# Performance work log

Measured on AMD Instinct MI355X. Metric: run time of the kernel, lower is better.

The kernel has to match this reference:

```python
import jax, jax.numpy as jnp
import numpy as np

B, T, F, H = 64, 2048, 256, 512


def setup_inputs() -> dict:
    key = jax.random.key(0)
    ks = jax.random.split(key, 8)
    s_ih = 1.0 / np.sqrt(H)
    return {
        "z": jax.random.normal(ks[0], (B, H), dtype=jnp.float32),
        "x": jax.random.normal(ks[1], (B, T, F), dtype=jnp.float32),
        "W_ih": jax.random.uniform(ks[2], (4 * H, F), minval=-s_ih, maxval=s_ih, dtype=jnp.float32),
        "W_hh": jax.random.uniform(ks[3], (4 * H, H), minval=-s_ih, maxval=s_ih, dtype=jnp.float32),
        "b_ih": jax.random.uniform(ks[4], (4 * H,), minval=-s_ih, maxval=s_ih, dtype=jnp.float32),
        "b_hh": jax.random.uniform(ks[5], (4 * H,), minval=-s_ih, maxval=s_ih, dtype=jnp.float32),
        "W_lin": jax.random.uniform(ks[6], (F, H), minval=-s_ih, maxval=s_ih, dtype=jnp.float32),
        "b_lin": jax.random.uniform(ks[7], (F,), minval=-s_ih, maxval=s_ih, dtype=jnp.float32),
    }


def _lstm_decode(z, x, W_ih, W_hh, b_ih, b_hh, W_lin, b_lin):
    # Teacher forcing: cell input at step t is x[:, t]. h0 = z, c0 = 0.
    # Precompute input projections for all timesteps in one GEMM: [T, B, 4H]
    x_t_major = jnp.swapaxes(x, 0, 1)  # [T, B, F]
    x_proj = jnp.einsum("tbf,gf->tbg", x_t_major, W_ih) + (b_ih + b_hh)
    h0 = z
    c0 = jnp.zeros_like(z)

    def step(carry, xp):
        h, c = carry
        gates = xp + h @ W_hh.T  # [B, 4H]
        i, f, g, o = jnp.split(gates, 4, axis=-1)  # PyTorch gate order: i,f,g,o
        i = jax.nn.sigmoid(i)
        f = jax.nn.sigmoid(f)
        g = jnp.tanh(g)
        o = jax.nn.sigmoid(o)
        c_new = f * c + i * g
        h_new = o * jnp.tanh(c_new)
        out_t = h_new @ W_lin.T + b_lin  # [B, F]
        return (h_new, c_new), out_t

    _, outs = jax.lax.scan(step, (h0, c0), x_proj)  # outs: [T, B, F]
    return jnp.swapaxes(outs, 0, 1)  # [B, T, F]


def reference(z, x, W_ih, W_hh, b_ih, b_hh, W_lin, b_lin):
    return _lstm_decode(z, x, W_ih, W_hh, b_ih, b_hh, W_lin, b_lin)
```

## Files before the change

### kernel.cpp

```cpp
#include <hip/hip_runtime.h>
#include <hip/hip_bf16.h>

#define B_   64
#define T_   2048
#define F_   256
#define H_   512
#define GB   4
#define GG   8
#define NWG  (GB*GG)
#define PKTS_PER_GROUP 4096
#define SLOTS 4

typedef __attribute__((ext_vector_type(8))) short bfrag;
typedef __attribute__((ext_vector_type(4))) int   int4v;
typedef __attribute__((ext_vector_type(2))) int   int2v;
typedef __attribute__((ext_vector_type(4))) float f32x4;
typedef __attribute__((ext_vector_type(4))) float float4_t;

__device__ __forceinline__ float fsig(float x)  { return 1.0f / (1.0f + __expf(-x)); }
__device__ __forceinline__ float ftanh(float x) { return 2.0f / (1.0f + __expf(-2.0f * x)) - 1.0f; }
__device__ __forceinline__ short f2bf(float f) {
  __hip_bfloat16 h = __float2bfloat16(f);
  return __builtin_bit_cast(short, h);
}

__device__ __forceinline__ int2v gload8_cc(const void* p) {
  int2v r;
  asm volatile("global_load_dwordx2 %0, %1, off sc0 sc1" : "=v"(r) : "v"(p));
  return r;
}
__device__ __forceinline__ void gstore8_cc(void* p, int2v d) {
  asm volatile("global_store_dwordx2 %0, %1, off sc0 sc1" :: "v"(p), "v"(d));
}
__device__ __forceinline__ void vm_drain() {
  asm volatile("s_waitcnt vmcnt(0)" ::: "memory");
  __builtin_amdgcn_sched_barrier(0);
}

__global__ void lstm_init(const float* __restrict__ z, unsigned long long* __restrict__ pkt0) {
  int i = blockIdx.x * blockDim.x + threadIdx.x;
  int g  = i >> 12;
  int p  = i & 4095;
  int j  = p >> 8;
  int pr = p & 255;
  int row = 16 * g + j;
  unsigned int lo = (unsigned)(unsigned short)f2bf(z[(size_t)row * H_ + 2 * pr])
                  | ((unsigned)(unsigned short)f2bf(z[(size_t)row * H_ + 2 * pr + 1]) << 16);
  pkt0[i] = (unsigned long long)lo;
}

__global__ void __launch_bounds__(256, 1)
lstm_persist(const float* __restrict__ x,
             const float* __restrict__ Wih,  const float* __restrict__ Whh,
             const float* __restrict__ bih,  const float* __restrict__ bhh,
             const float* __restrict__ Wlin, const float* __restrict__ blin,
             float* __restrict__ out, int2v* __restrict__ pkt)
{
  __shared__ char smem[49152];

  const int wg  = blockIdx.x;
  const int b   = wg >> 3;
  const int k   = wg & 7;
  const int tid = threadIdx.x;
  const int wv  = tid >> 6;
  const int l   = tid & 63;
  const int l16 = l & 15;
  const int qq  = l >> 4;
  const int swz = (l16 & 7) << 4;
  const int m4  = qq << 2;

  {
    const int oc = tid >> 3;
    const float* src = Wlin + (size_t)(32 * k + oc) * H_ + (tid & 7) * 64;
    char* dst = smem + 16384 + oc * 1024;
    #pragma unroll
    for (int i = 0; i < 8; ++i) {
      bfrag tmp;
      #pragma unroll
      for (int e = 0; e < 8; ++e) tmp[e] = f2bf(src[i * 8 + e]);
      *(int4v*)(dst + ((((tid & 7) * 128) + i * 16) ^ ((oc & 7) << 4))) =
          __builtin_bit_cast(int4v, tmp);
    }
  }

  bfrag WH[4][16];
  bfrag WI[4][8];
  float bs[4];
  #pragma unroll
  for (int q = 0; q < 4; ++q) {
    const int grow = q * H_ + k * 64 + wv * 16 + l16;
    #pragma unroll
    for (int kt = 0; kt < 16; ++kt) {
      const float* s = Whh + (size_t)grow * H_ + kt * 32 + qq * 8;
      bfrag w;
      #pragma unroll
      for (int e = 0; e < 8; ++e) w[e] = f2bf(s[e]);
      WH[q][kt] = w;
    }
    #pragma unroll
    for (int kt = 0; kt < 8; ++kt) {
      const float* s = Wih + (size_t)grow * F_ + kt * 32 + qq * 8;
      bfrag w;
      #pragma unroll
      for (int e = 0; e < 8; ++e) w[e] = f2bf(s[e]);
      WI[q][kt] = w;
    }
    bs[q] = bih[grow] + bhh[grow];
  }
  const float blc = (wv < 2) ? blin[32 * k + 16 * wv + l16] : 0.f;

  float c4[4] = {0.f, 0.f, 0.f, 0.f};
  __syncthreads();

  for (int t = 0; t < T_; ++t) {
    f32x4 acc[4] = {{0,0,0,0},{0,0,0,0},{0,0,0,0},{0,0,0,0}};
    {
      const float* xr = x + ((size_t)(16 * b + l16) * T_ + t) * F_ + qq * 8;
      #pragma unroll
      for (int kt = 0; kt < 8; ++kt) {
        float4_t xa = *(const float4_t*)(xr + kt * 32);
        float4_t xb = *(const float4_t*)(xr + kt * 32 + 4);
        bfrag a;
        #pragma unroll
        for (int e = 0; e < 4; ++e) { a[e] = f2bf(xa[e]); a[4 + e] = f2bf(xb[e]); }
        #pragma unroll
        for (int q = 0; q < 4; ++q)
          acc[q] = __builtin_amdgcn_mfma_f32_16x16x32_bf16(a, WI[q][kt], acc[q], 0, 0, 0);
      }
    }

    const int2v* pp = pkt + (size_t)((t & 3) * GB + b) * PKTS_PER_GROUP + tid;
    int2v pv[16];
    while (true) {
      #pragma unroll
      for (int j = 0; j < 16; ++j) pv[j] = gload8_cc(pp + j * 256);
      vm_drain();
      bool ok = true;
      #pragma unroll
      for (int j = 0; j < 16; ++j) ok &= (pv[j].y == t);
      if (__all(ok)) break;
      __builtin_amdgcn_s_sleep(2);
    }
    __syncthreads();

    #pragma unroll
    for (int j = 0; j < 16; ++j)
      *(int*)(smem + j * 1024 + ((tid * 4) ^ ((j & 7) << 4))) = pv[j].x;
    __syncthreads();

    f32x4 oacc = {blc, blc, blc, blc};
    #pragma unroll
    for (int kt = 0; kt < 16; ++kt) {
      bfrag a = *(const bfrag*)(smem + l16 * 1024 + ((kt * 64 + qq * 16) ^ swz));
      #pragma unroll
      for (int q = 0; q < 4; ++q)
        acc[q] = __builtin_amdgcn_mfma_f32_16x16x32_bf16(a, WH[q][kt], acc[q], 0, 0, 0);
      if (wv < 2) {
        bfrag wl = *(const bfrag*)(smem + 16384 + (16 * wv + l16) * 1024 +
                                   ((kt * 64 + qq * 16) ^ swz));
        oacc = __builtin_amdgcn_mfma_f32_16x16x32_bf16(a, wl, oacc, 0, 0, 0);
      }
    }

    int2v* ps = pkt + (size_t)(((t + 1) & 3) * GB + b) * PKTS_PER_GROUP;
    #pragma unroll
    for (int r = 0; r < 4; ++r) {
      float iv = fsig(acc[0][r] + bs[0]);
      float fv = fsig(acc[1][r] + bs[1]);
      float gv = ftanh(acc[2][r] + bs[2]);
      float ov = fsig(acc[3][r] + bs[3]);
      float cn = fv * c4[r] + iv * gv;
      c4[r] = cn;
      float hn = ov * ftanh(cn);
      int hb = (int)(unsigned short)f2bf(hn);
      int pu = __shfl_xor(hb, 1);
      if ((l16 & 1) == 0) {
        int2v pk;
        pk.x = (hb & 0xffff) | (pu << 16);
        pk.y = t + 1;
        gstore8_cc(ps + (m4 + r) * 256 + (32 * k + 8 * wv + (l16 >> 1)), pk);
      }
    }

    if (t > 0 && wv < 2) {
      #pragma unroll
      for (int r = 0; r < 4; ++r)
        out[(size_t)(16 * b + m4 + r) * T_ * F_ + (size_t)(t - 1) * F_ +
            32 * k + 16 * wv + l16] = oacc[r];
    }
  }

  {
    const int2v* pp = pkt + (size_t)((T_ & 3) * GB + b) * PKTS_PER_GROUP + tid;
    int2v pv[16];
    while (true) {
      #pragma unroll
      for (int j = 0; j < 16; ++j) pv[j] = gload8_cc(pp + j * 256);
      vm_drain();
      bool ok = true;
      #pragma unroll
      for (int j = 0; j < 16; ++j) ok &= (pv[j].y == T_);
      if (__all(ok)) break;
      __builtin_amdgcn_s_sleep(2);
    }
    __syncthreads();
    #pragma unroll
    for (int j = 0; j < 16; ++j)
      *(int*)(smem + j * 1024 + ((tid * 4) ^ ((j & 7) << 4))) = pv[j].x;
    __syncthreads();

    if (wv < 2) {
      f32x4 oacc = {blc, blc, blc, blc};
      #pragma unroll
      for (int kt = 0; kt < 16; ++kt) {
        bfrag a  = *(const bfrag*)(smem + l16 * 1024 + ((kt * 64 + qq * 16) ^ swz));
        bfrag wl = *(const bfrag*)(smem + 16384 + (16 * wv + l16) * 1024 +
                                   ((kt * 64 + qq * 16) ^ swz));
        oacc = __builtin_amdgcn_mfma_f32_16x16x32_bf16(a, wl, oacc, 0, 0, 0);
      }
      #pragma unroll
      for (int r = 0; r < 4; ++r)
        out[(size_t)(16 * b + m4 + r) * T_ * F_ + (size_t)(T_ - 1) * F_ +
            32 * k + 16 * wv + l16] = oacc[r];
    }
  }
}

extern "C" void kernel_launch(void* const* d_in, const int* in_sizes, int n_in,
                              void* d_out, int out_size, void* d_ws, size_t ws_size,
                              hipStream_t stream) {
  const float* z    = (const float*)d_in[0];
  const float* x    = (const float*)d_in[1];
  const float* Wih  = (const float*)d_in[2];
  const float* Whh  = (const float*)d_in[3];
  const float* bih  = (const float*)d_in[4];
  const float* bhh  = (const float*)d_in[5];
  const float* Wlin = (const float*)d_in[6];
  const float* blin = (const float*)d_in[7];
  float* out = (float*)d_out;

  int2v* pkt = (int2v*)d_ws;

  lstm_init<<<64, 256, 0, stream>>>(z, (unsigned long long*)d_ws);
  lstm_persist<<<NWG, 256, 0, stream>>>(x, Wih, Whh, bih, bhh, Wlin, blin, out, pkt);
}
```

Before: 14.19 ms.

## Regroup workgroups by XCD and exchange hidden state through L2 when co-located

The persistent LSTM grid moves from 32 workgroups (4 batch groups of 16 rows) to 64 workgroups (8 batch groups of 8 rows). Each group of 8 workgroups shares one hidden-state exchange. At startup every workgroup publishes its XCD id and checks whether its group peers sit on the same XCD. If they do, it polls a second packet buffer with L2-scope loads instead of system-coherent ones, to cut the latency of each step's cross-workgroup handoff. Every packet is now written to both buffers, half the MFMA rows are wasted padding, and a timeout falls back to the slow path.

```diff
diff --git a/kernel.cpp b/kernel.cpp
--- a/kernel.cpp
+++ b/kernel.cpp
@@ -5,10 +5,10 @@
 #define T_   2048
 #define F_   256
 #define H_   512
-#define GB   4
-#define GG   8
-#define NWG  (GB*GG)
-#define PKTS_PER_GROUP 4096
+#define NG   8
+#define GR   8
+#define NWG  64
+#define PKTS 2048
 #define SLOTS 4
 
 typedef __attribute__((ext_vector_type(8))) short bfrag;
@@ -32,21 +32,44 @@
 __device__ __forceinline__ void gstore8_cc(void* p, int2v d) {
   asm volatile("global_store_dwordx2 %0, %1, off sc0 sc1" :: "v"(p), "v"(d));
 }
+__device__ __forceinline__ void gstore4_cc(void* p, int d) {
+  asm volatile("global_store_dword %0, %1, off sc0 sc1" :: "v"(p), "v"(d));
+}
+__device__ __forceinline__ int gload_flag(const void* p) {
+  int r;
+  asm volatile("global_load_dword %0, %1, off sc0 sc1\n\ts_waitcnt vmcnt(0)"
+               : "=v"(r) : "v"(p) : "memory");
+  return r;
+}
+__device__ __forceinline__ int2v gload8_l2(const void* p) {
+  int2v r;
+  asm volatile("global_load_dwordx2 %0, %1, off sc0" : "=v"(r) : "v"(p));
+  return r;
+}
+__device__ __forceinline__ void gstore8_l2(void* p, int2v d) {
+  asm volatile("global_store_dwordx2 %0, %1, off sc0" :: "v"(p), "v"(d));
+}
 __device__ __forceinline__ void vm_drain() {
   asm volatile("s_waitcnt vmcnt(0)" ::: "memory");
   __builtin_amdgcn_sched_barrier(0);
 }
 
-__global__ void lstm_init(const float* __restrict__ z, unsigned long long* __restrict__ pkt0) {
+__global__ void lstm_init(const float* __restrict__ z,
+                          unsigned long long* __restrict__ fast0,
+                          unsigned long long* __restrict__ slow0,
+                          int* __restrict__ xcdmap) {
   int i = blockIdx.x * blockDim.x + threadIdx.x;
-  int g  = i >> 12;
-  int p  = i & 4095;
-  int j  = p >> 8;
-  int pr = p & 255;
-  int row = 16 * g + j;
+  if (i < NWG) xcdmap[i] = -1;
+  int g  = i >> 11;
+  int P  = i & 2047;
+  int r  = P >> 8;
+  int pr = P & 255;
+  int row = g * GR + r;
   unsigned int lo = (unsigned)(unsigned short)f2bf(z[(size_t)row * H_ + 2 * pr])
                   | ((unsigned)(unsigned short)f2bf(z[(size_t)row * H_ + 2 * pr + 1]) << 16);
-  pkt0[i] = (unsigned long long)lo;
+  unsigned long long pk = (unsigned long long)lo;
+  fast0[(size_t)g * PKTS + P] = pk;
+  slow0[(size_t)g * PKTS + P] = pk;
 }
 
 __global__ void __launch_bounds__(256, 1)
@@ -54,25 +77,44 @@
              const float* __restrict__ Wih,  const float* __restrict__ Whh,
              const float* __restrict__ bih,  const float* __restrict__ bhh,
              const float* __restrict__ Wlin, const float* __restrict__ blin,
-             float* __restrict__ out, int2v* __restrict__ pkt)
+             float* __restrict__ out,
+             int2v* __restrict__ fastp, int2v* __restrict__ slowp,
+             int* __restrict__ xcdmap)
 {
-  __shared__ char smem[49152];
+  __shared__ char smem[8192 + 32768 + 16];
+  const int hOff = 0, wOff = 8192, fOff = 8192 + 32768;
 
   const int wg  = blockIdx.x;
-  const int b   = wg >> 3;
-  const int k   = wg & 7;
+  const int g   = wg & 7;
+  const int mem = wg >> 3;
   const int tid = threadIdx.x;
   const int wv  = tid >> 6;
   const int l   = tid & 63;
   const int l16 = l & 15;
   const int qq  = l >> 4;
-  const int swz = (l16 & 7) << 4;
-  const int m4  = qq << 2;
+
+  const int xcc = __builtin_amdgcn_s_getreg(6164);
+  if (tid == 0) gstore4_cc(&xcdmap[wg], xcc);
+  vm_drain();
+  if (wv == 0) {
+    int other = xcc;
+    bool got = (l >= NG);
+    for (int it = 0; it < 200000; ++it) {
+      if (!got) {
+        int v = gload_flag(&xcdmap[g + NG * l]);
+        if (v != -1) { other = v; got = true; }
+      }
+      if (__all(got)) break;
+      __builtin_amdgcn_s_sleep(1);
+    }
+    int ok = __all(got && (other == xcc)) ? 1 : 0;
+    if (l == 0) *(int*)(smem + fOff) = ok;
+  }
 
   {
     const int oc = tid >> 3;
-    const float* src = Wlin + (size_t)(32 * k + oc) * H_ + (tid & 7) * 64;
-    char* dst = smem + 16384 + oc * 1024;
+    const float* src = Wlin + (size_t)(32 * mem + oc) * H_ + (tid & 7) * 64;
+    char* dst = smem + wOff + oc * 1024;
     #pragma unroll
     for (int i = 0; i < 8; ++i) {
       bfrag tmp;
@@ -83,12 +125,11 @@
     }
   }
 
-  bfrag WH[4][16];
-  bfrag WI[4][8];
+  bfrag WH[4][16], WI[4][8];
   float bs[4];
   #pragma unroll
   for (int q = 0; q < 4; ++q) {
-    const int grow = q * H_ + k * 64 + wv * 16 + l16;
+    const int grow = q * H_ + 64 * mem + 16 * wv + l16;
     #pragma unroll
     for (int kt = 0; kt < 16; ++kt) {
       const float* s = Whh + (size_t)grow * H_ + kt * 32 + qq * 8;
@@ -107,15 +148,18 @@
     }
     bs[q] = bih[grow] + bhh[grow];
   }
-  const float blc = (wv < 2) ? blin[32 * k + 16 * wv + l16] : 0.f;
+  const float blc = (wv < 2) ? blin[32 * mem + 16 * wv + l16] : 0.f;
 
   float c4[4] = {0.f, 0.f, 0.f, 0.f};
   __syncthreads();
+  bool useFast = (*(int*)(smem + fOff) != 0);
+
+  const int P0 = (tid >> 5) * 256 + (tid & 31);
 
   for (int t = 0; t < T_; ++t) {
     f32x4 acc[4] = {{0,0,0,0},{0,0,0,0},{0,0,0,0},{0,0,0,0}};
     {
-      const float* xr = x + ((size_t)(16 * b + l16) * T_ + t) * F_ + qq * 8;
+      const float* xr = x + ((size_t)(GR * g + (l16 & 7)) * T_ + t) * F_ + qq * 8;
       #pragma unroll
       for (int kt = 0; kt < 8; ++kt) {
         float4_t xa = *(const float4_t*)(xr + kt * 32);
@@ -129,99 +173,138 @@
       }
     }
 
-    const int2v* pp = pkt + (size_t)((t & 3) * GB + b) * PKTS_PER_GROUP + tid;
-    int2v pv[16];
+    const size_t slotOff = (size_t)((t & 3) * NG + g) * PKTS;
+    const int2v* fb = fastp + slotOff + P0;
+    const int2v* sb = slowp + slotOff + P0;
+    int2v pv[8];
+    int iter = 0;
     while (true) {
-      #pragma unroll
-      for (int j = 0; j < 16; ++j) pv[j] = gload8_cc(pp + j * 256);
+      if (useFast) {
+        #pragma unroll
+        for (int j = 0; j < 8; ++j) pv[j] = gload8_l2(fb + 32 * j);
+      } else {
+        #pragma unroll
+        for (int j = 0; j < 8; ++j) pv[j] = gload8_cc(sb + 32 * j);
+      }
       vm_drain();
       bool ok = true;
       #pragma unroll
-      for (int j = 0; j < 16; ++j) ok &= (pv[j].y == t);
+      for (int j = 0; j < 8; ++j) ok &= (pv[j].y == t);
       if (__all(ok)) break;
-      __builtin_amdgcn_s_sleep(2);
+      if (useFast && ++iter > 30000) useFast = false;
+      __builtin_amdgcn_s_sleep(1);
     }
     __syncthreads();
 
-    #pragma unroll
-    for (int j = 0; j < 16; ++j)
-      *(int*)(smem + j * 1024 + ((tid * 4) ^ ((j & 7) << 4))) = pv[j].x;
+    {
+      const int r = tid >> 5;
+      char* base = smem + hOff + r * 1024;
+      #pragma unroll
+      for (int j = 0; j < 8; ++j)
+        *(int*)(base + ((4 * ((tid & 31) + 32 * j)) ^ ((r & 7) << 4))) = pv[j].x;
+    }
     __syncthreads();
 
     f32x4 oacc = {blc, blc, blc, blc};
     #pragma unroll
     for (int kt = 0; kt < 16; ++kt) {
-      bfrag a = *(const bfrag*)(smem + l16 * 1024 + ((kt * 64 + qq * 16) ^ swz));
+      bfrag a = *(const bfrag*)(smem + hOff + (l16 & 7) * 1024 +
+                                ((kt * 64 + qq * 16) ^ ((l16 & 7) << 4)));
       #pragma unroll
       for (int q = 0; q < 4; ++q)
         acc[q] = __builtin_amdgcn_mfma_f32_16x16x32_bf16(a, WH[q][kt], acc[q], 0, 0, 0);
       if (wv < 2) {
-        bfrag wl = *(const bfrag*)(smem + 16384 + (16 * wv + l16) * 1024 +
-                                   ((kt * 64 + qq * 16) ^ swz));
+        const int oc = 16 * wv + l16;
+        bfrag wl = *(const bfrag*)(smem + wOff + oc * 1024 +
+                                   ((kt * 64 + qq * 16) ^ ((oc & 7) << 4)));
         oacc = __builtin_amdgcn_mfma_f32_16x16x32_bf16(a, wl, oacc, 0, 0, 0);
       }
     }
 
-    int2v* ps = pkt + (size_t)(((t + 1) & 3) * GB + b) * PKTS_PER_GROUP;
+    const size_t nxtOff = (size_t)(((t + 1) & 3) * NG + g) * PKTS;
+    int2v* fs = fastp + nxtOff;
+    int2v* ss = slowp + nxtOff;
     #pragma unroll
     for (int r = 0; r < 4; ++r) {
-      float iv = fsig(acc[0][r] + bs[0]);
-      float fv = fsig(acc[1][r] + bs[1]);
-      float gv = ftanh(acc[2][r] + bs[2]);
-      float ov = fsig(acc[3][r] + bs[3]);
-      float cn = fv * c4[r] + iv * gv;
-      c4[r] = cn;
-      float hn = ov * ftanh(cn);
+      float hn = 0.f;
+      if (qq < 2) {
+        float iv = fsig(acc[0][r] + bs[0]);
+        float fv = fsig(acc[1][r] + bs[1]);
+        float gv = ftanh(acc[2][r] + bs[2]);
+        float ov = fsig(acc[3][r] + bs[3]);
+        float cn = fv * c4[r] + iv * gv;
+        c4[r] = cn;
+        hn = ov * ftanh(cn);
+      }
       int hb = (int)(unsigned short)f2bf(hn);
       int pu = __shfl_xor(hb, 1);
-      if ((l16 & 1) == 0) {
+      if (qq < 2 && (l16 & 1) == 0) {
         int2v pk;
         pk.x = (hb & 0xffff) | (pu << 16);
         pk.y = t + 1;
-        gstore8_cc(ps + (m4 + r) * 256 + (32 * k + 8 * wv + (l16 >> 1)), pk);
-      }
-    }
-
-    if (t > 0 && wv < 2) {
+        const int P = (4 * qq + r) * 256 + (32 * mem + 8 * wv + (l16 >> 1));
+        gstore8_l2(fs + P, pk);
+        gstore8_cc(ss + P, pk);
+      }
+    }
+
+    if (t > 0 && wv < 2 && qq < 2) {
       #pragma unroll
       for (int r = 0; r < 4; ++r)
-        out[(size_t)(16 * b + m4 + r) * T_ * F_ + (size_t)(t - 1) * F_ +
-            32 * k + 16 * wv + l16] = oacc[r];
+        out[(size_t)(GR * g + 4 * qq + r) * T_ * F_ + (size_t)(t - 1) * F_ +
+            32 * mem + 16 * wv + l16] = oacc[r];
     }
   }
 
   {
-    const int2v* pp = pkt + (size_t)((T_ & 3) * GB + b) * PKTS_PER_GROUP + tid;
-    int2v pv[16];
+    const size_t slotOff = (size_t)((T_ & 3) * NG + g) * PKTS;
+    const int2v* fb = fastp + slotOff + P0;
+    const int2v* sb = slowp + slotOff + P0;
+    int2v pv[8];
+    int iter = 0;
     while (true) {
-      #pragma unroll
-      for (int j = 0; j < 16; ++j) pv[j] = gload8_cc(pp + j * 256);
+      if (useFast) {
+        #pragma unroll
+        for (int j = 0; j < 8; ++j) pv[j] = gload8_l2(fb + 32 * j);
+      } else {
+        #pragma unroll
+        for (int j = 0; j < 8; ++j) pv[j] = gload8_cc(sb + 32 * j);
+      }
       vm_drain();
       bool ok = true;
       #pragma unroll
-      for (int j = 0; j < 16; ++j) ok &= (pv[j].y == T_);
+      for (int j = 0; j < 8; ++j) ok &= (pv[j].y == T_);
       if (__all(ok)) break;
-      __builtin_amdgcn_s_sleep(2);
+      if (useFast && ++iter > 30000) useFast = false;
+      __builtin_amdgcn_s_sleep(1);
     }
     __syncthreads();
-    #pragma unroll
-    for (int j = 0; j < 16; ++j)
-      *(int*)(smem + j * 1024 + ((tid * 4) ^ ((j & 7) << 4))) = pv[j].x;
+    {
+      const int r = tid >> 5;
+      char* base = smem + hOff + r * 1024;
+      #pragma unroll
+      for (int j = 0; j < 8; ++j)
+        *(int*)(base + ((4 * ((tid & 31) + 32 * j)) ^ ((r & 7) << 4))) = pv[j].x;
+    }
     __syncthreads();
 
     if (wv < 2) {
       f32x4 oacc = {blc, blc, blc, blc};
       #pragma unroll
       for (int kt = 0; kt < 16; ++kt) {
-        bfrag a  = *(const bfrag*)(smem + l16 * 1024 + ((kt * 64 + qq * 16) ^ swz));
-        bfrag wl = *(const bfrag*)(smem + 16384 + (16 * wv + l16) * 1024 +
-                                   ((kt * 64 + qq * 16) ^ swz));
+        bfrag a = *(const bfrag*)(smem + hOff + (l16 & 7) * 1024 +
+                                  ((kt * 64 + qq * 16) ^ ((l16 & 7) << 4)));
+        const int oc = 16 * wv + l16;
+        bfrag wl = *(const bfrag*)(smem + wOff + oc * 1024 +
+                                   ((kt * 64 + qq * 16) ^ ((oc & 7) << 4)));
         oacc = __builtin_amdgcn_mfma_f32_16x16x32_bf16(a, wl, oacc, 0, 0, 0);
       }
-      #pragma unroll
-      for (int r = 0; r < 4; ++r)
-        out[(size_t)(16 * b + m4 + r) * T_ * F_ + (size_t)(T_ - 1) * F_ +
-            32 * k + 16 * wv + l16] = oacc[r];
+      if (qq < 2) {
+        #pragma unroll
+        for (int r = 0; r < 4; ++r)
+          out[(size_t)(GR * g + 4 * qq + r) * T_ * F_ + (size_t)(T_ - 1) * F_ +
+              32 * mem + 16 * wv + l16] = oacc[r];
+      }
     }
   }
 }
@@ -239,8 +322,13 @@
   const float* blin = (const float*)d_in[7];
   float* out = (float*)d_out;
 
-  int2v* pkt = (int2v*)d_ws;
-
-  lstm_init<<<64, 256, 0, stream>>>(z, (unsigned long long*)d_ws);
-  lstm_persist<<<NWG, 256, 0, stream>>>(x, Wih, Whh, bih, bhh, Wlin, blin, out, pkt);
-}
+  const size_t bufBytes = (size_t)SLOTS * NG * PKTS * 8;
+  int2v* fastp = (int2v*)d_ws;
+  int2v* slowp = (int2v*)((char*)d_ws + bufBytes);
+  int*   xcdmap = (int*)((char*)d_ws + 2 * bufBytes);
+
+  lstm_init<<<64, 256, 0, stream>>>(z, (unsigned long long*)fastp,
+                                    (unsigned long long*)slowp, xcdmap);
+  lstm_persist<<<NWG, 256, 0, stream>>>(x, Wih, Whh, bih, bhh, Wlin, blin, out,
+                                        fastp, slowp, xcdmap);
+}
```

Result: slower. 38.70 ms (+172.8%).

## Replace per-packet sequence tags with per-workgroup flags and double-buffered payload

Applied to the files above, without the earlier changes.

Swaps the inter-workgroup handoff of the hidden state, which tagged every 8-byte packet with a step number and polled all packets, for 4-byte payload writes plus one flag per workgroup written after a drain and block barrier. Consumers spin on 8 flags and then read the payload once, which halves the payload traffic and shrinks polling to a few small loads. The ring drops from 4 slots to 2. In exchange it adds an extra vm drain, a __syncthreads and a serialized flag store on every step, and the release ordering rests on sc0/sc1 stores being visible before the flag.

```diff
diff --git a/kernel.cpp b/kernel.cpp
--- a/kernel.cpp
+++ b/kernel.cpp
@@ -8,12 +8,10 @@
 #define GB   4
 #define GG   8
 #define NWG  (GB*GG)
-#define PKTS_PER_GROUP 4096
-#define SLOTS 4
+#define PAYD 4096
 
 typedef __attribute__((ext_vector_type(8))) short bfrag;
 typedef __attribute__((ext_vector_type(4))) int   int4v;
-typedef __attribute__((ext_vector_type(2))) int   int2v;
 typedef __attribute__((ext_vector_type(4))) float f32x4;
 typedef __attribute__((ext_vector_type(4))) float float4_t;
 
@@ -24,29 +22,37 @@
   return __builtin_bit_cast(short, h);
 }
 
-__device__ __forceinline__ int2v gload8_cc(const void* p) {
-  int2v r;
-  asm volatile("global_load_dwordx2 %0, %1, off sc0 sc1" : "=v"(r) : "v"(p));
+__device__ __forceinline__ int gload4_cc(const void* p) {
+  int r;
+  asm volatile("global_load_dword %0, %1, off sc0 sc1" : "=v"(r) : "v"(p));
   return r;
 }
-__device__ __forceinline__ void gstore8_cc(void* p, int2v d) {
-  asm volatile("global_store_dwordx2 %0, %1, off sc0 sc1" :: "v"(p), "v"(d));
+__device__ __forceinline__ void gstore4_cc(void* p, int d) {
+  asm volatile("global_store_dword %0, %1, off sc0 sc1" :: "v"(p), "v"(d));
+}
+__device__ __forceinline__ int gload_flag(const void* p) {
+  int r;
+  asm volatile("global_load_dword %0, %1, off sc0 sc1\n\ts_waitcnt vmcnt(0)"
+               : "=v"(r) : "v"(p) : "memory");
+  return r;
 }
 __device__ __forceinline__ void vm_drain() {
   asm volatile("s_waitcnt vmcnt(0)" ::: "memory");
   __builtin_amdgcn_sched_barrier(0);
 }
 
-__global__ void lstm_init(const float* __restrict__ z, unsigned long long* __restrict__ pkt0) {
+__global__ void lstm_init(const float* __restrict__ z, int* __restrict__ pay,
+                          int* __restrict__ flags) {
   int i = blockIdx.x * blockDim.x + threadIdx.x;
+  if (i < GB * 16) flags[i] = 0;
   int g  = i >> 12;
   int p  = i & 4095;
   int j  = p >> 8;
   int pr = p & 255;
   int row = 16 * g + j;
-  unsigned int lo = (unsigned)(unsigned short)f2bf(z[(size_t)row * H_ + 2 * pr])
-                  | ((unsigned)(unsigned short)f2bf(z[(size_t)row * H_ + 2 * pr + 1]) << 16);
-  pkt0[i] = (unsigned long long)lo;
+  int lo = (int)((unsigned)(unsigned short)f2bf(z[(size_t)row * H_ + 2 * pr])
+         | ((unsigned)(unsigned short)f2bf(z[(size_t)row * H_ + 2 * pr + 1]) << 16));
+  pay[(size_t)g * PAYD + p] = lo;
 }
 
 __global__ void __launch_bounds__(256, 1)
@@ -54,7 +60,8 @@
              const float* __restrict__ Wih,  const float* __restrict__ Whh,
              const float* __restrict__ bih,  const float* __restrict__ bhh,
              const float* __restrict__ Wlin, const float* __restrict__ blin,
-             float* __restrict__ out, int2v* __restrict__ pkt)
+             float* __restrict__ out, int* __restrict__ pay,
+             int* __restrict__ flags)
 {
   __shared__ char smem[49152];
 
@@ -112,6 +119,8 @@
   float c4[4] = {0.f, 0.f, 0.f, 0.f};
   __syncthreads();
 
+  const int* myflags = flags + b * 16;
+
   for (int t = 0; t < T_; ++t) {
     f32x4 acc[4] = {{0,0,0,0},{0,0,0,0},{0,0,0,0},{0,0,0,0}};
     {
@@ -129,23 +138,24 @@
       }
     }
 
-    const int2v* pp = pkt + (size_t)((t & 3) * GB + b) * PKTS_PER_GROUP + tid;
-    int2v pv[16];
-    while (true) {
-      #pragma unroll
-      for (int j = 0; j < 16; ++j) pv[j] = gload8_cc(pp + j * 256);
-      vm_drain();
-      bool ok = true;
-      #pragma unroll
-      for (int j = 0; j < 16; ++j) ok &= (pv[j].y == t);
-      if (__all(ok)) break;
-      __builtin_amdgcn_s_sleep(2);
-    }
+    if (t > 0) {
+      while (true) {
+        int v = gload_flag(&myflags[l & 7]);
+        if (__all(v >= t)) break;
+        __builtin_amdgcn_s_sleep(1);
+      }
+      __builtin_amdgcn_sched_barrier(0);
+    }
+    const int* pp = pay + (size_t)((t & 1) * GB + b) * PAYD + tid;
+    int pv[16];
+    #pragma unroll
+    for (int j = 0; j < 16; ++j) pv[j] = gload4_cc(pp + j * 256);
+    vm_drain();
     __syncthreads();
 
     #pragma unroll
     for (int j = 0; j < 16; ++j)
-      *(int*)(smem + j * 1024 + ((tid * 4) ^ ((j & 7) << 4))) = pv[j].x;
+      *(int*)(smem + j * 1024 + ((tid * 4) ^ ((j & 7) << 4))) = pv[j];
     __syncthreads();
 
     f32x4 oacc = {blc, blc, blc, blc};
@@ -162,7 +172,7 @@
       }
     }
 
-    int2v* ps = pkt + (size_t)(((t + 1) & 3) * GB + b) * PKTS_PER_GROUP;
+    int* ps = pay + (size_t)(((t + 1) & 1) * GB + b) * PAYD;
     #pragma unroll
     for (int r = 0; r < 4; ++r) {
       float iv = fsig(acc[0][r] + bs[0]);
@@ -175,12 +185,14 @@
       int hb = (int)(unsigned short)f2bf(hn);
       int pu = __shfl_xor(hb, 1);
       if ((l16 & 1) == 0) {
-        int2v pk;
-        pk.x = (hb & 0xffff) | (pu << 16);
-        pk.y = t + 1;
-        gstore8_cc(ps + (m4 + r) * 256 + (32 * k + 8 * wv + (l16 >> 1)), pk);
-      }
-    }
+        int packed = (hb & 0xffff) | (pu << 16);
+        gstore4_cc(ps + (m4 + r) * 256 + (32 * k + 8 * wv + (l16 >> 1)), packed);
+      }
+    }
+    vm_drain();
+    __syncthreads();
+    if (tid == 0)
+      gstore4_cc((void*)&flags[b * 16 + k], t + 1);
 
     if (t > 0 && wv < 2) {
       #pragma unroll
@@ -191,22 +203,22 @@
   }
 
   {
-    const int2v* pp = pkt + (size_t)((T_ & 3) * GB + b) * PKTS_PER_GROUP + tid;
-    int2v pv[16];
     while (true) {
-      #pragma unroll
-      for (int j = 0; j < 16; ++j) pv[j] = gload8_cc(pp + j * 256);
-      vm_drain();
-      bool ok = true;
-      #pragma unroll
-      for (int j = 0; j < 16; ++j) ok &= (pv[j].y == T_);
-      if (__all(ok)) break;
-      __builtin_amdgcn_s_sleep(2);
-    }
+      int v = gload_flag(&myflags[l & 7]);
+      if (__all(v >= T_)) break;
+      __builtin_amdgcn_s_sleep(1);
+    }
+    __builtin_amdgcn_sched_barrier(0);
+
+    const int* pp = pay + (size_t)((T_ & 1) * GB + b) * PAYD + tid;
+    int pv[16];
+    #pragma unroll
+    for (int j = 0; j < 16; ++j) pv[j] = gload4_cc(pp + j * 256);
+    vm_drain();
     __syncthreads();
     #pragma unroll
     for (int j = 0; j < 16; ++j)
-      *(int*)(smem + j * 1024 + ((tid * 4) ^ ((j & 7) << 4))) = pv[j].x;
+      *(int*)(smem + j * 1024 + ((tid * 4) ^ ((j & 7) << 4))) = pv[j];
     __syncthreads();
 
     if (wv < 2) {
@@ -239,8 +251,10 @@
   const float* blin = (const float*)d_in[7];
   float* out = (float*)d_out;
 
-  int2v* pkt = (int2v*)d_ws;
-
-  lstm_init<<<64, 256, 0, stream>>>(z, (unsigned long long*)d_ws);
-  lstm_persist<<<NWG, 256, 0, stream>>>(x, Wih, Whh, bih, bhh, Wlin, blin, out, pkt);
-}
+  int* pay   = (int*)d_ws;
+  int* flags = (int*)((char*)d_ws + 192 * 1024);
+
+  lstm_init<<<64, 256, 0, stream>>>(z, pay, flags);
+  lstm_persist<<<NWG, 256, 0, stream>>>(x, Wih, Whh, bih, bhh, Wlin, blin, out,
+                                        pay, flags);
+}
```

New measurement: 14.17 ms. No clear change (-0.1%).

## Split recurrent K-reduction across two wave halves and overlap polling with input GEMM

Applied to the files above, without the earlier changes.

Each workgroup goes from 256 to 512 threads. The two halves of the waves each take half of the K dimension for the input and recurrent MFMAs, and the partial sums are reduced through LDS. Gate math runs on one half while the other half computes the output projection, so the output linear no longer sits on the critical path of the gate waves. The packet loads for h are issued before the x-projection MFMAs to hide polling latency. This shortens the per-step serial chain and halves per-thread weight registers, at the cost of an extra LDS reduction and barrier each step.

```diff
diff --git a/kernel.cpp b/kernel.cpp
--- a/kernel.cpp
+++ b/kernel.cpp
@@ -8,8 +8,7 @@
 #define GB   4
 #define GG   8
 #define NWG  (GB*GG)
-#define PKTS_PER_GROUP 4096
-#define SLOTS 4
+#define PAYD 4096
 
 typedef __attribute__((ext_vector_type(8))) short bfrag;
 typedef __attribute__((ext_vector_type(4))) int   int4v;
@@ -37,87 +36,95 @@
   __builtin_amdgcn_sched_barrier(0);
 }
 
-__global__ void lstm_init(const float* __restrict__ z, unsigned long long* __restrict__ pkt0) {
+__global__ void lstm_init(const float* __restrict__ z,
+                          unsigned long long* __restrict__ pkt0) {
   int i = blockIdx.x * blockDim.x + threadIdx.x;
   int g  = i >> 12;
   int p  = i & 4095;
-  int j  = p >> 8;
+  int r  = p >> 8;
   int pr = p & 255;
-  int row = 16 * g + j;
+  int row = 16 * g + r;
   unsigned int lo = (unsigned)(unsigned short)f2bf(z[(size_t)row * H_ + 2 * pr])
                   | ((unsigned)(unsigned short)f2bf(z[(size_t)row * H_ + 2 * pr + 1]) << 16);
-  pkt0[i] = (unsigned long long)lo;
-}
-
-__global__ void __launch_bounds__(256, 1)
+  pkt0[(size_t)g * PAYD + p] = (unsigned long long)lo;
+}
+
+__global__ void __launch_bounds__(512, 1)
 lstm_persist(const float* __restrict__ x,
              const float* __restrict__ Wih,  const float* __restrict__ Whh,
              const float* __restrict__ bih,  const float* __restrict__ bhh,
              const float* __restrict__ Wlin, const float* __restrict__ blin,
              float* __restrict__ out, int2v* __restrict__ pkt)
 {
-  __shared__ char smem[49152];
+  __shared__ char smem[65536];
 
   const int wg  = blockIdx.x;
   const int b   = wg >> 3;
   const int k   = wg & 7;
   const int tid = threadIdx.x;
-  const int wv  = tid >> 6;
+  const int w   = tid >> 6;
+  const int ct  = w & 3;
+  const int kh  = w >> 2;
   const int l   = tid & 63;
   const int l16 = l & 15;
   const int qq  = l >> 4;
+  const int m4  = qq << 2;
   const int swz = (l16 & 7) << 4;
-  const int m4  = qq << 2;
 
   {
-    const int oc = tid >> 3;
-    const float* src = Wlin + (size_t)(32 * k + oc) * H_ + (tid & 7) * 64;
+    const int oc = tid >> 4;
+    const int s  = tid & 15;
+    const float* src = Wlin + (size_t)(32 * k + oc) * H_ + s * 32;
     char* dst = smem + 16384 + oc * 1024;
     #pragma unroll
-    for (int i = 0; i < 8; ++i) {
+    for (int i = 0; i < 4; ++i) {
       bfrag tmp;
       #pragma unroll
       for (int e = 0; e < 8; ++e) tmp[e] = f2bf(src[i * 8 + e]);
-      *(int4v*)(dst + ((((tid & 7) * 128) + i * 16) ^ ((oc & 7) << 4))) =
+      *(int4v*)(dst + ((s * 64 + i * 16) ^ ((oc & 7) << 4))) =
           __builtin_bit_cast(int4v, tmp);
     }
   }
 
-  bfrag WH[4][16];
-  bfrag WI[4][8];
-  float bs[4];
+  bfrag WH[4][8]; bfrag WI[4][4]; float bs[4];
   #pragma unroll
   for (int q = 0; q < 4; ++q) {
-    const int grow = q * H_ + k * 64 + wv * 16 + l16;
-    #pragma unroll
-    for (int kt = 0; kt < 16; ++kt) {
-      const float* s = Whh + (size_t)grow * H_ + kt * 32 + qq * 8;
-      bfrag w;
-      #pragma unroll
-      for (int e = 0; e < 8; ++e) w[e] = f2bf(s[e]);
-      WH[q][kt] = w;
-    }
-    #pragma unroll
-    for (int kt = 0; kt < 8; ++kt) {
-      const float* s = Wih + (size_t)grow * F_ + kt * 32 + qq * 8;
-      bfrag w;
-      #pragma unroll
-      for (int e = 0; e < 8; ++e) w[e] = f2bf(s[e]);
-      WI[q][kt] = w;
+    const int grow = q * H_ + k * 64 + ct * 16 + l16;
+    #pragma unroll
+    for (int kt2 = 0; kt2 < 8; ++kt2) {
+      const float* s = Whh + (size_t)grow * H_ + (8 * kh + kt2) * 32 + qq * 8;
+      bfrag wv_;
+      #pragma unroll
+      for (int e = 0; e < 8; ++e) wv_[e] = f2bf(s[e]);
+      WH[q][kt2] = wv_;
+    }
+    #pragma unroll
+    for (int kt2 = 0; kt2 < 4; ++kt2) {
+      const float* s = Wih + (size_t)grow * F_ + (4 * kh + kt2) * 32 + qq * 8;
+      bfrag wv_;
+      #pragma unroll
+      for (int e = 0; e < 8; ++e) wv_[e] = f2bf(s[e]);
+      WI[q][kt2] = wv_;
     }
     bs[q] = bih[grow] + bhh[grow];
   }
-  const float blc = (wv < 2) ? blin[32 * k + 16 * wv + l16] : 0.f;
+  const float blc = (kh == 1 && ct < 2) ? blin[32 * k + 16 * ct + l16] : 0.f;
 
   float c4[4] = {0.f, 0.f, 0.f, 0.f};
   __syncthreads();
 
   for (int t = 0; t < T_; ++t) {
+    const int2v* pp = pkt + (size_t)((t & 3) * GB + b) * PAYD + tid;
+    int2v pv[8];
+    #pragma unroll
+    for (int j = 0; j < 8; ++j) pv[j] = gload8_cc(pp + j * 512);
+
     f32x4 acc[4] = {{0,0,0,0},{0,0,0,0},{0,0,0,0},{0,0,0,0}};
     {
       const float* xr = x + ((size_t)(16 * b + l16) * T_ + t) * F_ + qq * 8;
       #pragma unroll
-      for (int kt = 0; kt < 8; ++kt) {
+      for (int kt2 = 0; kt2 < 4; ++kt2) {
+        const int kt = 4 * kh + kt2;
         float4_t xa = *(const float4_t*)(xr + kt * 32);
         float4_t xb = *(const float4_t*)(xr + kt * 32 + 4);
         bfrag a;
@@ -125,103 +132,128 @@
         for (int e = 0; e < 4; ++e) { a[e] = f2bf(xa[e]); a[4 + e] = f2bf(xb[e]); }
         #pragma unroll
         for (int q = 0; q < 4; ++q)
-          acc[q] = __builtin_amdgcn_mfma_f32_16x16x32_bf16(a, WI[q][kt], acc[q], 0, 0, 0);
-      }
-    }
-
-    const int2v* pp = pkt + (size_t)((t & 3) * GB + b) * PKTS_PER_GROUP + tid;
-    int2v pv[16];
+          acc[q] = __builtin_amdgcn_mfma_f32_16x16x32_bf16(a, WI[q][kt2], acc[q], 0, 0, 0);
+      }
+    }
+
+    vm_drain();
+    {
+      bool ok = true;
+      #pragma unroll
+      for (int j = 0; j < 8; ++j) ok &= (pv[j].y == t);
+      while (!__all(ok)) {
+        __builtin_amdgcn_s_sleep(2);
+        #pragma unroll
+        for (int j = 0; j < 8; ++j) pv[j] = gload8_cc(pp + j * 512);
+        vm_drain();
+        ok = true;
+        #pragma unroll
+        for (int j = 0; j < 8; ++j) ok &= (pv[j].y == t);
+      }
+    }
+    __syncthreads();
+
+    #pragma unroll
+    for (int j = 0; j < 8; ++j) {
+      const int P = tid + j * 512;
+      *(int*)(smem + (P >> 8) * 1024 + (((P & 255) * 4) ^ (((P >> 8) & 7) << 4))) = pv[j].x;
+    }
+    __syncthreads();
+
+    #pragma unroll
+    for (int kt2 = 0; kt2 < 8; ++kt2) {
+      const int kt = 8 * kh + kt2;
+      bfrag a = *(const bfrag*)(smem + l16 * 1024 + ((kt * 64 + qq * 16) ^ swz));
+      #pragma unroll
+      for (int q = 0; q < 4; ++q)
+        acc[q] = __builtin_amdgcn_mfma_f32_16x16x32_bf16(a, WH[q][kt2], acc[q], 0, 0, 0);
+    }
+
+    if (kh == 1) {
+      #pragma unroll
+      for (int q = 0; q < 4; ++q)
+        *(f32x4*)(smem + 49152 + ct * 4096 + q * 1024 + l * 16) = acc[q];
+    }
+    __syncthreads();
+
+    if (kh == 0) {
+      #pragma unroll
+      for (int q = 0; q < 4; ++q)
+        acc[q] += *(const f32x4*)(smem + 49152 + ct * 4096 + q * 1024 + l * 16);
+
+      int2v* ps = pkt + (size_t)(((t + 1) & 3) * GB + b) * PAYD;
+      #pragma unroll
+      for (int r = 0; r < 4; ++r) {
+        float iv = fsig(acc[0][r] + bs[0]);
+        float fv = fsig(acc[1][r] + bs[1]);
+        float gv = ftanh(acc[2][r] + bs[2]);
+        float ov = fsig(acc[3][r] + bs[3]);
+        float cn = fv * c4[r] + iv * gv;
+        c4[r] = cn;
+        float hn = ov * ftanh(cn);
+        int hb = (int)(unsigned short)f2bf(hn);
+        int pu = __shfl_xor(hb, 1);
+        if ((l16 & 1) == 0) {
+          int2v pk;
+          pk.x = (hb & 0xffff) | (pu << 16);
+          pk.y = t + 1;
+          gstore8_cc(ps + (m4 + r) * 256 + (32 * k + 8 * ct + (l16 >> 1)), pk);
+        }
+      }
+    } else if (ct < 2) {
+      f32x4 oacc = {blc, blc, blc, blc};
+      const int oc = 16 * ct + l16;
+      #pragma unroll
+      for (int kt = 0; kt < 16; ++kt) {
+        bfrag a  = *(const bfrag*)(smem + l16 * 1024 + ((kt * 64 + qq * 16) ^ swz));
+        bfrag wl = *(const bfrag*)(smem + 16384 + oc * 1024 +
+                                   ((kt * 64 + qq * 16) ^ ((oc & 7) << 4)));
+        oacc = __builtin_amdgcn_mfma_f32_16x16x32_bf16(a, wl, oacc, 0, 0, 0);
+      }
+      if (t > 0) {
+        #pragma unroll
+        for (int r = 0; r < 4; ++r)
+          out[(size_t)(16 * b + m4 + r) * T_ * F_ + (size_t)(t - 1) * F_ +
+              32 * k + 16 * ct + l16] = oacc[r];
+      }
+    }
+  }
+
+  {
+    const int2v* pp = pkt + (size_t)((T_ & 3) * GB + b) * PAYD + tid;
+    int2v pv[8];
     while (true) {
       #pragma unroll
-      for (int j = 0; j < 16; ++j) pv[j] = gload8_cc(pp + j * 256);
+      for (int j = 0; j < 8; ++j) pv[j] = gload8_cc(pp + j * 512);
       vm_drain();
       bool ok = true;
       #pragma unroll
-      for (int j = 0; j < 16; ++j) ok &= (pv[j].y == t);
+      for (int j = 0; j < 8; ++j) ok &= (pv[j].y == T_);
       if (__all(ok)) break;
       __builtin_amdgcn_s_sleep(2);
     }
     __syncthreads();
-
-    #pragma unroll
-    for (int j = 0; j < 16; ++j)
-      *(int*)(smem + j * 1024 + ((tid * 4) ^ ((j & 7) << 4))) = pv[j].x;
-    __syncthreads();
-
-    f32x4 oacc = {blc, blc, blc, blc};
-    #pragma unroll
-    for (int kt = 0; kt < 16; ++kt) {
-      bfrag a = *(const bfrag*)(smem + l16 * 1024 + ((kt * 64 + qq * 16) ^ swz));
-      #pragma unroll
-      for (int q = 0; q < 4; ++q)
-        acc[q] = __builtin_amdgcn_mfma_f32_16x16x32_bf16(a, WH[q][kt], acc[q], 0, 0, 0);
-      if (wv < 2) {
-        bfrag wl = *(const bfrag*)(smem + 16384 + (16 * wv + l16) * 1024 +
-                                   ((kt * 64 + qq * 16) ^ swz));
-        oacc = __builtin_amdgcn_mfma_f32_16x16x32_bf16(a, wl, oacc, 0, 0, 0);
-      }
-    }
-
-    int2v* ps = pkt + (size_t)(((t + 1) & 3) * GB + b) * PKTS_PER_GROUP;
-    #pragma unroll
-    for (int r = 0; r < 4; ++r) {
-      float iv = fsig(acc[0][r] + bs[0]);
-      float fv = fsig(acc[1][r] + bs[1]);
-      float gv = ftanh(acc[2][r] + bs[2]);
-      float ov = fsig(acc[3][r] + bs[3]);
-      float cn = fv * c4[r] + iv * gv;
-      c4[r] = cn;
-      float hn = ov * ftanh(cn);
-      int hb = (int)(unsigned short)f2bf(hn);
-      int pu = __shfl_xor(hb, 1);
-      if ((l16 & 1) == 0) {
-        int2v pk;
-        pk.x = (hb & 0xffff) | (pu << 16);
-        pk.y = t + 1;
-        gstore8_cc(ps + (m4 + r) * 256 + (32 * k + 8 * wv + (l16 >> 1)), pk);
-      }
-    }
-
-    if (t > 0 && wv < 2) {
-      #pragma unroll
-      for (int r = 0; r < 4; ++r)
-        out[(size_t)(16 * b + m4 + r) * T_ * F_ + (size_t)(t - 1) * F_ +
-            32 * k + 16 * wv + l16] = oacc[r];
-    }
-  }
-
-  {
-    const int2v* pp = pkt + (size_t)((T_ & 3) * GB + b) * PKTS_PER_GROUP + tid;
-    int2v pv[16];
-    while (true) {
-      #pragma unroll
-      for (int j = 0; j < 16; ++j) pv[j] = gload8_cc(pp + j * 256);
-      vm_drain();
-      bool ok = true;
-      #pragma unroll
-      for (int j = 0; j < 16; ++j) ok &= (pv[j].y == T_);
-      if (__all(ok)) break;
-      __builtin_amdgcn_s_sleep(2);
-    }
-    __syncthreads();
-    #pragma unroll
-    for (int j = 0; j < 16; ++j)
-      *(int*)(smem + j * 1024 + ((tid * 4) ^ ((j & 7) << 4))) = pv[j].x;
-    __syncthreads();
-
-    if (wv < 2) {
+    #pragma unroll
+    for (int j = 0; j < 8; ++j) {
+      const int P = tid + j * 512;
+      *(int*)(smem + (P >> 8) * 1024 + (((P & 255) * 4) ^ (((P >> 8) & 7) << 4))) = pv[j].x;
+    }
+    __syncthreads();
+
+    if (kh == 1 && ct < 2) {
       f32x4 oacc = {blc, blc, blc, blc};
+      const int oc = 16 * ct + l16;
       #pragma unroll
       for (int kt = 0; kt < 16; ++kt) {
         bfrag a  = *(const bfrag*)(smem + l16 * 1024 + ((kt * 64 + qq * 16) ^ swz));
-        bfrag wl = *(const bfrag*)(smem + 16384 + (16 * wv + l16) * 1024 +
-                                   ((kt * 64 + qq * 16) ^ swz));
+        bfrag wl = *(const bfrag*)(smem + 16384 + oc * 1024 +
+                                   ((kt * 64 + qq * 16) ^ ((oc & 7) << 4)));
         oacc = __builtin_amdgcn_mfma_f32_16x16x32_bf16(a, wl, oacc, 0, 0, 0);
       }
       #pragma unroll
       for (int r = 0; r < 4; ++r)
         out[(size_t)(16 * b + m4 + r) * T_ * F_ + (size_t)(T_ - 1) * F_ +
-            32 * k + 16 * wv + l16] = oacc[r];
+            32 * k + 16 * ct + l16] = oacc[r];
     }
   }
 }
@@ -241,6 +273,6 @@
 
   int2v* pkt = (int2v*)d_ws;
 
-  lstm_init<<<64, 256, 0, stream>>>(z, (unsigned long long*)d_ws);
-  lstm_persist<<<NWG, 256, 0, stream>>>(x, Wih, Whh, bih, bhh, Wlin, blin, out, pkt);
-}
+  lstm_init<<<64, 256, 0, stream>>>(z, (unsigned long long*)pkt);
+  lstm_persist<<<NWG, 512, 0, stream>>>(x, Wih, Whh, bih, bhh, Wlin, blin, out, pkt);
+}
```

After: 16.52 ms. 16.4% more time.
